# Performance work log

Measured on AMD Instinct MI355X. Metric: run time of the kernel, lower is better.

The kernel has to match this reference:

```python
import jax, jax.numpy as jnp
import numpy as np

NUM_HEADS = 12
HIDDEN = 768
HEAD = HIDDEN // NUM_HEADS
B, N = 16, 512


def setup_inputs() -> dict:
    key = jax.random.key(0)
    ks = jax.random.split(key, 9)
    s = 0.02
    return {
        "x": jax.random.normal(ks[0], (B, N, HIDDEN), jnp.float32),
        "spatial_encoding": jax.random.normal(ks[1], (B, N, N), jnp.float32),
        "edge_encoding": jax.random.normal(ks[2], (B, N, N), jnp.float32),
        "Wq": jax.random.normal(ks[3], (HIDDEN, HIDDEN), jnp.float32) * s,
        "Wk": jax.random.normal(ks[4], (HIDDEN, HIDDEN), jnp.float32) * s,
        "Wv": jax.random.normal(ks[5], (HIDDEN, HIDDEN), jnp.float32) * s,
        "bv": jax.random.normal(ks[6], (HIDDEN,), jnp.float32) * s,
        "Wo": jax.random.normal(ks[7], (HIDDEN, HIDDEN), jnp.float32) * s,
        "bo": jax.random.normal(ks[8], (HIDDEN,), jnp.float32) * s,
    }


def reference(x, spatial_encoding, edge_encoding, Wq, Wk, Wv, bv, Wo, bo):
    b, n, h = x.shape
    scale = jnp.asarray(HIDDEN, x.dtype) ** -0.5  # note: hidden_dim, not head_size
    # projections (torch Linear: x @ W.T + b), split heads -> (b, n, nh, hd)
    q = (x @ Wq.T).reshape(b, n, NUM_HEADS, HEAD)
    k = (x @ Wk.T).reshape(b, n, NUM_HEADS, HEAD)
    v = (x @ Wv.T + bv).reshape(b, n, NUM_HEADS, HEAD)
    bias = (spatial_encoding + edge_encoding)[:, None]  # (b, 1, n, n)
    scores = jnp.einsum("bqhd,bkhd->bhqk", q, k) * scale + bias  # (b, nh, n, n)
    # rows that are entirely zero get masked to -inf, then nan_to_num after softmax
    row_nonzero = jnp.any(scores != 0, axis=-1, keepdims=True)
    scores = jnp.where(row_nonzero, scores, -jnp.inf)
    p = jax.nn.softmax(scores, axis=-1)
    p = jnp.nan_to_num(p)
    out = jnp.einsum("bhqk,bkhd->bqhd", p, v).reshape(b, n, h)
    # dropout is identity in eval mode
    return out @ Wo.T + bo
```

## Files before the change

kernel.cpp:

```cpp
#include <hip/hip_runtime.h>

typedef unsigned short u16;
typedef short bf16x8 __attribute__((ext_vector_type(8)));
typedef short bf16x4 __attribute__((ext_vector_type(4)));
typedef float f32x4 __attribute__((ext_vector_type(4)));
typedef unsigned u32x4 __attribute__((ext_vector_type(4)));
typedef unsigned short u16x4 __attribute__((ext_vector_type(4)));

#define HID 768
#define NH  12
#define HD  64
#define BB  16
#define SEQ 512
#define TOK (BB*SEQ)

static __device__ __forceinline__ u16 f2bf(float f){
  union { float f; unsigned u; } x; x.f = f;
  unsigned r = x.u + 0x7fffu + ((x.u >> 16) & 1u);
  return (u16)(r >> 16);
}
static __device__ __forceinline__ float bf2f(u16 h){
  return __builtin_bit_cast(float, ((unsigned)h) << 16);
}

static __device__ __forceinline__ void gl_lds16(const void* g, void* l){
  __builtin_amdgcn_global_load_lds(
      (const __attribute__((address_space(1))) unsigned int*)g,
      (__attribute__((address_space(3))) unsigned int*)l, 16, 0, 0);
}

__global__ __launch_bounds__(256, 4) void k_convert(
    const float* __restrict__ x,  const float* __restrict__ sp,
    const float* __restrict__ ed, const float* __restrict__ wq,
    const float* __restrict__ wk, const float* __restrict__ wv,
    const float* __restrict__ wo,
    u16* __restrict__ xbf, u16* __restrict__ wqkv, u16* __restrict__ wob,
    u16* __restrict__ bsumb)
{
  const int NQX = TOK*HID/4;
  const int NQW = 3*HID*HID/4;
  const int NQO = HID*HID/4;
  int idx = blockIdx.x*256 + threadIdx.x;
  if (idx < NQX){
    int e = idx*4;
    float4 v = *(const float4*)(x+e);
    ushort4 o; o.x=f2bf(v.x); o.y=f2bf(v.y); o.z=f2bf(v.z); o.w=f2bf(v.w);
    *(ushort4*)(xbf+e) = o;
  } else if (idx < NQX+NQW){
    int e = (idx-NQX)*4;
    int row = e/HID, col = e%HID;
    const float* w = (row<768) ? (wq+row*HID)
                   : (row<1536 ? wk+(row-768)*HID : wv+(row-1536)*HID);
    float4 v = *(const float4*)(w+col);
    ushort4 o; o.x=f2bf(v.x); o.y=f2bf(v.y); o.z=f2bf(v.z); o.w=f2bf(v.w);
    *(ushort4*)(wqkv+e) = o;
  } else if (idx < NQX+NQW+NQO){
    int e = (idx-NQX-NQW)*4;
    float4 v = *(const float4*)(wo+e);
    ushort4 o; o.x=f2bf(v.x); o.y=f2bf(v.y); o.z=f2bf(v.z); o.w=f2bf(v.w);
    *(ushort4*)(wob+e) = o;
  } else {
    int e = (idx-NQX-NQW-NQO)*4;
    float4 a = *(const float4*)(sp+e);
    float4 b = *(const float4*)(ed+e);
    ushort4 o; o.x=f2bf(a.x+b.x); o.y=f2bf(a.y+b.y);
               o.z=f2bf(a.z+b.z); o.w=f2bf(a.w+b.w);
    *(ushort4*)(bsumb+e) = o;
  }
}

template<int MODE>
__global__ __launch_bounds__(256, 2) void k_gemm(
    const u16* __restrict__ A, const u16* __restrict__ Bt,
    const float* __restrict__ bias,
    u16* __restrict__ o16a, u16* __restrict__ o16b,
    float* __restrict__ outf)
{
  __shared__ u16 As[2][128*32];
  __shared__ u16 Bs[2][128*32];
  const int tid = threadIdx.x;
  const int wid = tid >> 6, lane = tid & 63;
  const int g = lane >> 4, c = lane & 15;
  const int wr = wid >> 1, wc = wid & 1;
  const long mbase = (long)blockIdx.y * 128;
  const int  nbase = blockIdx.x * 128;

  f32x4 acc[4][4];
  #pragma unroll
  for (int i=0;i<4;i++)
    #pragma unroll
    for (int j=0;j<4;j++){ f32x4 z = {0.f,0.f,0.f,0.f}; acc[i][j] = z; }

  const char* Abase = (const char*)A  + mbase * HID * 2;
  const char* Bbase = (const char*)Bt + (long)nbase * HID * 2;

  const int L0 = wid*1024 + lane*16;
  const int ar0 = L0 >> 6, ai0 = L0 & 63;
  const int L1 = L0 + 4096;
  const int ar1 = L1 >> 6, ai1 = L1 & 63;

  #define STAGE(buf, kk) do { \
    gl_lds16(Abase + (long)ar0*1536 + (kk)*2 + ai0, (char*)As[buf] + wid*1024); \
    gl_lds16(Abase + (long)ar1*1536 + (kk)*2 + ai1, (char*)As[buf] + 4096 + wid*1024); \
    gl_lds16(Bbase + (long)ar0*1536 + (kk)*2 + ai0, (char*)Bs[buf] + wid*1024); \
    gl_lds16(Bbase + (long)ar1*1536 + (kk)*2 + ai1, (char*)Bs[buf] + 4096 + wid*1024); \
  } while(0)

  STAGE(0, 0);
  __syncthreads();

  #pragma unroll 2
  for (int t = 0; t < 24; t++){
    if (t < 23) STAGE((t+1)&1, (t+1)*32);
    const char* Ab = (const char*)As[t&1];
    const char* Bb = (const char*)Bs[t&1];
    bf16x8 af[4], bfr[4];
    #pragma unroll
    for (int mt=0; mt<4; mt++){
      int row = wr*64 + mt*16 + c;
      af[mt] = *(const bf16x8*)(Ab + row*64 + g*16);
    }
    #pragma unroll
    for (int nt=0; nt<4; nt++){
      int row = wc*64 + nt*16 + c;
      bfr[nt] = *(const bf16x8*)(Bb + row*64 + g*16);
    }
    #pragma unroll
    for (int mt=0; mt<4; mt++)
      #pragma unroll
      for (int nt=0; nt<4; nt++)
        acc[mt][nt] = __builtin_amdgcn_mfma_f32_16x16x32_bf16(
            af[mt], bfr[nt], acc[mt][nt], 0,0,0);
    __syncthreads();
  }
  #undef STAGE

  if constexpr (MODE == 1){
    #pragma unroll
    for (int nt=0; nt<4; nt++){
      int colg = nbase + wc*64 + nt*16 + c;
      float bb = bias[colg];
      #pragma unroll
      for (int mt=0; mt<4; mt++)
        #pragma unroll
        for (int r=0;r<4;r++){
          long rowg = mbase + wr*64 + mt*16 + g*4 + r;
          outf[rowg*HID + colg] = acc[mt][nt][r] + bb;
        }
    }
  } else if constexpr (MODE == 0){
    int region = blockIdx.x / 6;
    #pragma unroll
    for (int nt=0; nt<4; nt++){
      int colg = nbase + wc*64 + nt*16 + c;
      int o = colg - region*768;
      int h = o >> 6, dd = o & 63;
      #pragma unroll
      for (int mt=0; mt<4; mt++)
        #pragma unroll
        for (int r=0;r<4;r++){
          long rowg = mbase + wr*64 + mt*16 + g*4 + r;
          int b = (int)(rowg >> 9), n = (int)(rowg & 511);
          long hb = (long)(b*NH + h);
          u16 val = f2bf(acc[mt][nt][r]);
          if (region==0) o16a[(hb*SEQ + n)*HD + dd] = val;
          else           o16b[(hb*SEQ + n)*HD + dd] = val;
        }
    }
  } else {
    #pragma unroll
    for (int mt=0; mt<4; mt++){
      int rowg0 = (int)mbase + wr*64 + mt*16 + g*4;
      float4 bb = *(const float4*)(bias + rowg0);
      #pragma unroll
      for (int r=0;r<4;r++){
        int rowg = rowg0 + r;
        int h = rowg >> 6, dd = rowg & 63;
        float bv_ = r==0?bb.x : r==1?bb.y : r==2?bb.z : bb.w;
        #pragma unroll
        for (int nt=0; nt<4; nt++){
          int colg = nbase + wc*64 + nt*16 + c;
          int b = colg >> 9, n = colg & 511;
          o16a[((long)(b*NH + h)*HD + dd)*SEQ + n] = f2bf(acc[mt][nt][r] + bv_);
        }
      }
    }
  }
}

__global__ __launch_bounds__(256, 4) void k_attn(
    const u16* __restrict__ Qh, const u16* __restrict__ Kh,
    const u16* __restrict__ VTh, const u16* __restrict__ bsumb,
    u16* __restrict__ attn)
{
  __shared__ u16 Ks[2][64*64];
  __shared__ u16 Vs[2][64*64];

  const int tid = threadIdx.x;
  const int wid = tid>>6, lane = tid&63, g = lane>>4, c = lane&15;
  const int L = (blockIdx.x & 7)*192 + (blockIdx.x >> 3);
  const int qt = L & 7, h = (L>>3) % 12, b = L/96;
  const u16*  Qp = Qh + (long)(b*NH+h)*SEQ*HD;
  const char* Kp = (const char*)(Kh  + (long)(b*NH+h)*SEQ*HD);
  const char* Vp = (const char*)(VTh + (long)(b*NH+h)*HD*SEQ);
  const int qbase = qt*64 + wid*16;

  bf16x8 qf0 = *(const bf16x8*)(Qp + (qbase + c)*HD +  0 + g*8);
  bf16x8 qf1 = *(const bf16x8*)(Qp + (qbase + c)*HD + 32 + g*8);

  const float scale = 0.036084391824351615f;
  const u16* bp = bsumb + (long)b*SEQ*SEQ + (long)(qbase + c)*SEQ + g*4;

  const int s0 = tid*16;
  const int r0 = s0>>7, i0 = (s0&127) ^ ((r0&7)<<4);
  const int s1 = s0 + 4096;
  const int r1 = s1>>7, i1 = (s1&127) ^ ((r1&7)<<4);

  #define STAGE(buf, ch) do { \
    gl_lds16(Kp + (long)((ch)*64 + r0)*128 + i0, (char*)Ks[buf] + wid*1024); \
    gl_lds16(Kp + (long)((ch)*64 + r1)*128 + i1, (char*)Ks[buf] + wid*1024 + 4096); \
    gl_lds16(Vp + (long)r0*1024 + (ch)*128 + i0, (char*)Vs[buf] + wid*1024); \
    gl_lds16(Vp + (long)r1*1024 + (ch)*128 + i1, (char*)Vs[buf] + wid*1024 + 4096); \
  } while(0)

  f32x4 o[4];
  #pragma unroll
  for (int dt=0;dt<4;dt++){ f32x4 z = {0.f,0.f,0.f,0.f}; o[dt]=z; }
  float l = 0.f;

  STAGE(0, 0);
  __syncthreads();

  #pragma unroll
  for (int ch=0; ch<8; ch++){
    if (ch < 7) STAGE((ch+1)&1, ch+1);
    const char* Kb = (const char*)Ks[ch&1];
    const char* Vb = (const char*)Vs[ch&1];
    const u16* bpc = bp + ch*64;
    u16x4 rb0 = *(const u16x4*)(bpc);
    u16x4 rb1 = *(const u16x4*)(bpc + 16);
    u16x4 rb2 = *(const u16x4*)(bpc + 32);
    u16x4 rb3 = *(const u16x4*)(bpc + 48);
    #pragma unroll
    for (int s=0; s<2; s++){
      const u16x4 rA = s ? rb2 : rb0;
      const u16x4 rB = s ? rb3 : rb1;
      const int rAi = s*32 + c, rBi = s*32 + 16 + c;
      const int mA = (rAi&7)<<4, mB = (rBi&7)<<4;
      bf16x8 ka0 = *(const bf16x8*)(Kb + rAi*128 + ((   g*16) ^ mA));
      bf16x8 ka1 = *(const bf16x8*)(Kb + rAi*128 + ((64+g*16) ^ mA));
      bf16x8 kb0 = *(const bf16x8*)(Kb + rBi*128 + ((   g*16) ^ mB));
      bf16x8 kb1 = *(const bf16x8*)(Kb + rBi*128 + ((64+g*16) ^ mB));
      f32x4 sA = {0.f,0.f,0.f,0.f}, sB = {0.f,0.f,0.f,0.f};
      sA = __builtin_amdgcn_mfma_f32_16x16x32_bf16(ka0, qf0, sA, 0,0,0);
      sA = __builtin_amdgcn_mfma_f32_16x16x32_bf16(ka1, qf1, sA, 0,0,0);
      sB = __builtin_amdgcn_mfma_f32_16x16x32_bf16(kb0, qf0, sB, 0,0,0);
      sB = __builtin_amdgcn_mfma_f32_16x16x32_bf16(kb1, qf1, sB, 0,0,0);
      float pA0 = __expf(fmaf(sA[0], scale, bf2f(rA[0])));
      float pA1 = __expf(fmaf(sA[1], scale, bf2f(rA[1])));
      float pA2 = __expf(fmaf(sA[2], scale, bf2f(rA[2])));
      float pA3 = __expf(fmaf(sA[3], scale, bf2f(rA[3])));
      float pB0 = __expf(fmaf(sB[0], scale, bf2f(rB[0])));
      float pB1 = __expf(fmaf(sB[1], scale, bf2f(rB[1])));
      float pB2 = __expf(fmaf(sB[2], scale, bf2f(rB[2])));
      float pB3 = __expf(fmaf(sB[3], scale, bf2f(rB[3])));
      l += ((pA0 + pA1) + (pA2 + pA3)) + ((pB0 + pB1) + (pB2 + pB3));
      u32x4 paw = { (unsigned)f2bf(pA0) | ((unsigned)f2bf(pA1) << 16),
                    (unsigned)f2bf(pA2) | ((unsigned)f2bf(pA3) << 16),
                    (unsigned)f2bf(pB0) | ((unsigned)f2bf(pB1) << 16),
                    (unsigned)f2bf(pB2) | ((unsigned)f2bf(pB3) << 16) };
      bf16x8 pav = __builtin_bit_cast(bf16x8, paw);
      #pragma unroll
      for (int dt=0; dt<4; dt++){
        const int vr = dt*16 + c, mV = (vr&7)<<4;
        bf16x4 v0 = *(const bf16x4*)(Vb + vr*128 + ((s*64    + g*8) ^ mV));
        bf16x4 v1 = *(const bf16x4*)(Vb + vr*128 + ((s*64+32 + g*8) ^ mV));
        bf16x8 vbv = __builtin_shufflevector(v0, v1, 0,1,2,3,4,5,6,7);
        o[dt] = __builtin_amdgcn_mfma_f32_16x16x32_bf16(pav, vbv, o[dt], 0,0,0);
      }
    }
    __syncthreads();
  }
  #undef STAGE

  l += __shfl_xor(l, 16, 64);
  l += __shfl_xor(l, 32, 64);
  float linv = 1.f / l;

  #pragma unroll
  for (int r=0;r<4;r++){
    float li = __shfl(linv, g*4 + r, 64);
    int q = qbase + g*4 + r;
    #pragma unroll
    for (int dt=0; dt<4; dt++)
      attn[(long)(b*SEQ + q)*HID + h*64 + dt*16 + c] = f2bf(o[dt][r] * li);
  }
}

extern "C" void kernel_launch(void* const* d_in, const int* in_sizes, int n_in,
                              void* d_out, int out_size, void* d_ws, size_t ws_size,
                              hipStream_t stream)
{
  const float* x  = (const float*)d_in[0];
  const float* sp = (const float*)d_in[1];
  const float* ed = (const float*)d_in[2];
  const float* Wq = (const float*)d_in[3];
  const float* Wk = (const float*)d_in[4];
  const float* Wv = (const float*)d_in[5];
  const float* bv = (const float*)d_in[6];
  const float* Wo = (const float*)d_in[7];
  const float* bo = (const float*)d_in[8];
  float* out = (float*)d_out;

  u16* w = (u16*)d_ws;
  u16* xbf  = w;
  u16* wqkv = xbf  + TOK*HID;
  u16* wob  = wqkv + 3*HID*HID;
  u16* qh   = wob  + HID*HID;
  u16* kh   = qh   + TOK*HID;
  u16* vth  = kh   + TOK*HID;
  u16* attn = vth  + TOK*HID;
  u16* bsumb = attn + TOK*HID;

  k_convert<<<12544, 256, 0, stream>>>(x, sp, ed, Wq, Wk, Wv, Wo,
                                       xbf, wqkv, wob, bsumb);
  dim3 gQK(12, 64);
  k_gemm<0><<<gQK, 256, 0, stream>>>(xbf, wqkv, nullptr, qh, kh, nullptr);
  dim3 gVT(64, 6);
  k_gemm<2><<<gVT, 256, 0, stream>>>(wqkv + 2*HID*HID, xbf, bv, vth, nullptr, nullptr);
  k_attn<<<1536, 256, 0, stream>>>(qh, kh, vth, bsumb, attn);
  dim3 gO(6, 64);
  k_gemm<1><<<gO, 256, 0, stream>>>(attn, wob, bo, nullptr, nullptr, out);
}
```

Baseline: 146.7 us.

## Process two query tiles per attention block to reuse K/V LDS tiles

Each attention block now handles 128 query rows instead of 64, with each wave computing two 16-row query groups that share the same K and V fragments loaded from LDS. This halves the number of blocks and halves the global K/V staging traffic per query, and it amortizes the LDS reads across twice the MFMA work. In exchange it raises register pressure, so launch bounds drop to 3 blocks per CU, and with 768 blocks there is less parallelism to hide latency.

New measurement: 155.3 us. 1.06x slower.

```diff
diff --git a/kernel.cpp b/kernel.cpp
--- a/kernel.cpp
+++ b/kernel.cpp
@@ -188,7 +188,7 @@
   }
 }
 
-__global__ __launch_bounds__(256, 4) void k_attn(
+__global__ __launch_bounds__(256, 3) void k_attn(
     const u16* __restrict__ Qh, const u16* __restrict__ Kh,
     const u16* __restrict__ VTh, const u16* __restrict__ bsumb,
     u16* __restrict__ attn)
@@ -198,18 +198,22 @@
 
   const int tid = threadIdx.x;
   const int wid = tid>>6, lane = tid&63, g = lane>>4, c = lane&15;
-  const int L = (blockIdx.x & 7)*192 + (blockIdx.x >> 3);
-  const int qt = L & 7, h = (L>>3) % 12, b = L/96;
+  const int L = (blockIdx.x & 7)*96 + (blockIdx.x >> 3);
+  const int qt2 = L & 3, h = (L>>2) % 12, b = L/48;
   const u16*  Qp = Qh + (long)(b*NH+h)*SEQ*HD;
   const char* Kp = (const char*)(Kh  + (long)(b*NH+h)*SEQ*HD);
   const char* Vp = (const char*)(VTh + (long)(b*NH+h)*HD*SEQ);
-  const int qbase = qt*64 + wid*16;
-
-  bf16x8 qf0 = *(const bf16x8*)(Qp + (qbase + c)*HD +  0 + g*8);
-  bf16x8 qf1 = *(const bf16x8*)(Qp + (qbase + c)*HD + 32 + g*8);
+  const int qb0 = qt2*128 + wid*16;
+  const int qb1 = qb0 + 64;
+
+  bf16x8 qA0 = *(const bf16x8*)(Qp + (qb0 + c)*HD +  0 + g*8);
+  bf16x8 qA1 = *(const bf16x8*)(Qp + (qb0 + c)*HD + 32 + g*8);
+  bf16x8 qB0 = *(const bf16x8*)(Qp + (qb1 + c)*HD +  0 + g*8);
+  bf16x8 qB1 = *(const bf16x8*)(Qp + (qb1 + c)*HD + 32 + g*8);
 
   const float scale = 0.036084391824351615f;
-  const u16* bp = bsumb + (long)b*SEQ*SEQ + (long)(qbase + c)*SEQ + g*4;
+  const u16* bp0 = bsumb + (long)b*SEQ*SEQ + (long)(qb0 + c)*SEQ + g*4;
+  const u16* bp1 = bp0 + 64*SEQ;
 
   const int s0 = tid*16;
   const int r0 = s0>>7, i0 = (s0&127) ^ ((r0&7)<<4);
@@ -223,10 +227,10 @@
     gl_lds16(Vp + (long)r1*1024 + (ch)*128 + i1, (char*)Vs[buf] + wid*1024 + 4096); \
   } while(0)
 
-  f32x4 o[4];
+  f32x4 o0[4], o1[4];
   #pragma unroll
-  for (int dt=0;dt<4;dt++){ f32x4 z = {0.f,0.f,0.f,0.f}; o[dt]=z; }
-  float l = 0.f;
+  for (int dt=0;dt<4;dt++){ f32x4 z = {0.f,0.f,0.f,0.f}; o0[dt]=z; o1[dt]=z; }
+  float l0 = 0.f, l1 = 0.f;
 
   STAGE(0, 0);
   __syncthreads();
@@ -236,64 +240,92 @@
     if (ch < 7) STAGE((ch+1)&1, ch+1);
     const char* Kb = (const char*)Ks[ch&1];
     const char* Vb = (const char*)Vs[ch&1];
-    const u16* bpc = bp + ch*64;
-    u16x4 rb0 = *(const u16x4*)(bpc);
-    u16x4 rb1 = *(const u16x4*)(bpc + 16);
-    u16x4 rb2 = *(const u16x4*)(bpc + 32);
-    u16x4 rb3 = *(const u16x4*)(bpc + 48);
+    const u16* bpc0 = bp0 + ch*64;
+    const u16* bpc1 = bp1 + ch*64;
+    u16x4 ra0 = *(const u16x4*)(bpc0);      u16x4 ra1 = *(const u16x4*)(bpc0+16);
+    u16x4 ra2 = *(const u16x4*)(bpc0+32);   u16x4 ra3 = *(const u16x4*)(bpc0+48);
+    u16x4 rc0 = *(const u16x4*)(bpc1);      u16x4 rc1 = *(const u16x4*)(bpc1+16);
+    u16x4 rc2 = *(const u16x4*)(bpc1+32);   u16x4 rc3 = *(const u16x4*)(bpc1+48);
     #pragma unroll
     for (int s=0; s<2; s++){
-      const u16x4 rA = s ? rb2 : rb0;
-      const u16x4 rB = s ? rb3 : rb1;
+      const u16x4 bA0 = s ? ra2 : ra0;
+      const u16x4 bB0 = s ? ra3 : ra1;
+      const u16x4 bA1 = s ? rc2 : rc0;
+      const u16x4 bB1 = s ? rc3 : rc1;
       const int rAi = s*32 + c, rBi = s*32 + 16 + c;
       const int mA = (rAi&7)<<4, mB = (rBi&7)<<4;
       bf16x8 ka0 = *(const bf16x8*)(Kb + rAi*128 + ((   g*16) ^ mA));
       bf16x8 ka1 = *(const bf16x8*)(Kb + rAi*128 + ((64+g*16) ^ mA));
       bf16x8 kb0 = *(const bf16x8*)(Kb + rBi*128 + ((   g*16) ^ mB));
       bf16x8 kb1 = *(const bf16x8*)(Kb + rBi*128 + ((64+g*16) ^ mB));
-      f32x4 sA = {0.f,0.f,0.f,0.f}, sB = {0.f,0.f,0.f,0.f};
-      sA = __builtin_amdgcn_mfma_f32_16x16x32_bf16(ka0, qf0, sA, 0,0,0);
-      sA = __builtin_amdgcn_mfma_f32_16x16x32_bf16(ka1, qf1, sA, 0,0,0);
-      sB = __builtin_amdgcn_mfma_f32_16x16x32_bf16(kb0, qf0, sB, 0,0,0);
-      sB = __builtin_amdgcn_mfma_f32_16x16x32_bf16(kb1, qf1, sB, 0,0,0);
-      float pA0 = __expf(fmaf(sA[0], scale, bf2f(rA[0])));
-      float pA1 = __expf(fmaf(sA[1], scale, bf2f(rA[1])));
-      float pA2 = __expf(fmaf(sA[2], scale, bf2f(rA[2])));
-      float pA3 = __expf(fmaf(sA[3], scale, bf2f(rA[3])));
-      float pB0 = __expf(fmaf(sB[0], scale, bf2f(rB[0])));
-      float pB1 = __expf(fmaf(sB[1], scale, bf2f(rB[1])));
-      float pB2 = __expf(fmaf(sB[2], scale, bf2f(rB[2])));
-      float pB3 = __expf(fmaf(sB[3], scale, bf2f(rB[3])));
-      l += ((pA0 + pA1) + (pA2 + pA3)) + ((pB0 + pB1) + (pB2 + pB3));
-      u32x4 paw = { (unsigned)f2bf(pA0) | ((unsigned)f2bf(pA1) << 16),
+      f32x4 sA0={0.f,0.f,0.f,0.f}, sB0={0.f,0.f,0.f,0.f};
+      f32x4 sA1={0.f,0.f,0.f,0.f}, sB1={0.f,0.f,0.f,0.f};
+      sA0 = __builtin_amdgcn_mfma_f32_16x16x32_bf16(ka0, qA0, sA0, 0,0,0);
+      sA0 = __builtin_amdgcn_mfma_f32_16x16x32_bf16(ka1, qA1, sA0, 0,0,0);
+      sB0 = __builtin_amdgcn_mfma_f32_16x16x32_bf16(kb0, qA0, sB0, 0,0,0);
+      sB0 = __builtin_amdgcn_mfma_f32_16x16x32_bf16(kb1, qA1, sB0, 0,0,0);
+      sA1 = __builtin_amdgcn_mfma_f32_16x16x32_bf16(ka0, qB0, sA1, 0,0,0);
+      sA1 = __builtin_amdgcn_mfma_f32_16x16x32_bf16(ka1, qB1, sA1, 0,0,0);
+      sB1 = __builtin_amdgcn_mfma_f32_16x16x32_bf16(kb0, qB0, sB1, 0,0,0);
+      sB1 = __builtin_amdgcn_mfma_f32_16x16x32_bf16(kb1, qB1, sB1, 0,0,0);
+      float pA0 = __expf(fmaf(sA0[0], scale, bf2f(bA0[0])));
+      float pA1 = __expf(fmaf(sA0[1], scale, bf2f(bA0[1])));
+      float pA2 = __expf(fmaf(sA0[2], scale, bf2f(bA0[2])));
+      float pA3 = __expf(fmaf(sA0[3], scale, bf2f(bA0[3])));
+      float pB0 = __expf(fmaf(sB0[0], scale, bf2f(bB0[0])));
+      float pB1 = __expf(fmaf(sB0[1], scale, bf2f(bB0[1])));
+      float pB2 = __expf(fmaf(sB0[2], scale, bf2f(bB0[2])));
+      float pB3 = __expf(fmaf(sB0[3], scale, bf2f(bB0[3])));
+      l0 += ((pA0 + pA1) + (pA2 + pA3)) + ((pB0 + pB1) + (pB2 + pB3));
+      u32x4 pw0 = { (unsigned)f2bf(pA0) | ((unsigned)f2bf(pA1) << 16),
                     (unsigned)f2bf(pA2) | ((unsigned)f2bf(pA3) << 16),
                     (unsigned)f2bf(pB0) | ((unsigned)f2bf(pB1) << 16),
                     (unsigned)f2bf(pB2) | ((unsigned)f2bf(pB3) << 16) };
-      bf16x8 pav = __builtin_bit_cast(bf16x8, paw);
+      bf16x8 pav0 = __builtin_bit_cast(bf16x8, pw0);
+      float qA0f = __expf(fmaf(sA1[0], scale, bf2f(bA1[0])));
+      float qA1f = __expf(fmaf(sA1[1], scale, bf2f(bA1[1])));
+      float qA2f = __expf(fmaf(sA1[2], scale, bf2f(bA1[2])));
+      float qA3f = __expf(fmaf(sA1[3], scale, bf2f(bA1[3])));
+      float qB0f = __expf(fmaf(sB1[0], scale, bf2f(bB1[0])));
+      float qB1f = __expf(fmaf(sB1[1], scale, bf2f(bB1[1])));
+      float qB2f = __expf(fmaf(sB1[2], scale, bf2f(bB1[2])));
+      float qB3f = __expf(fmaf(sB1[3], scale, bf2f(bB1[3])));
+      l1 += ((qA0f + qA1f) + (qA2f + qA3f)) + ((qB0f + qB1f) + (qB2f + qB3f));
+      u32x4 pw1 = { (unsigned)f2bf(qA0f) | ((unsigned)f2bf(qA1f) << 16),
+                    (unsigned)f2bf(qA2f) | ((unsigned)f2bf(qA3f) << 16),
+                    (unsigned)f2bf(qB0f) | ((unsigned)f2bf(qB1f) << 16),
+                    (unsigned)f2bf(qB2f) | ((unsigned)f2bf(qB3f) << 16) };
+      bf16x8 pav1 = __builtin_bit_cast(bf16x8, pw1);
       #pragma unroll
       for (int dt=0; dt<4; dt++){
         const int vr = dt*16 + c, mV = (vr&7)<<4;
         bf16x4 v0 = *(const bf16x4*)(Vb + vr*128 + ((s*64    + g*8) ^ mV));
         bf16x4 v1 = *(const bf16x4*)(Vb + vr*128 + ((s*64+32 + g*8) ^ mV));
         bf16x8 vbv = __builtin_shufflevector(v0, v1, 0,1,2,3,4,5,6,7);
-        o[dt] = __builtin_amdgcn_mfma_f32_16x16x32_bf16(pav, vbv, o[dt], 0,0,0);
+        o0[dt] = __builtin_amdgcn_mfma_f32_16x16x32_bf16(pav0, vbv, o0[dt], 0,0,0);
+        o1[dt] = __builtin_amdgcn_mfma_f32_16x16x32_bf16(pav1, vbv, o1[dt], 0,0,0);
       }
     }
     __syncthreads();
   }
   #undef STAGE
 
-  l += __shfl_xor(l, 16, 64);
-  l += __shfl_xor(l, 32, 64);
-  float linv = 1.f / l;
+  l0 += __shfl_xor(l0, 16, 64);
+  l0 += __shfl_xor(l0, 32, 64);
+  l1 += __shfl_xor(l1, 16, 64);
+  l1 += __shfl_xor(l1, 32, 64);
+  float li0 = 1.f / l0, li1 = 1.f / l1;
 
   #pragma unroll
   for (int r=0;r<4;r++){
-    float li = __shfl(linv, g*4 + r, 64);
-    int q = qbase + g*4 + r;
-    #pragma unroll
-    for (int dt=0; dt<4; dt++)
-      attn[(long)(b*SEQ + q)*HID + h*64 + dt*16 + c] = f2bf(o[dt][r] * li);
+    float u0 = __shfl(li0, g*4 + r, 64);
+    float u1 = __shfl(li1, g*4 + r, 64);
+    int q0 = qb0 + g*4 + r, q1 = qb1 + g*4 + r;
+    #pragma unroll
+    for (int dt=0; dt<4; dt++){
+      attn[(long)(b*SEQ + q0)*HID + h*64 + dt*16 + c] = f2bf(o0[dt][r] * u0);
+      attn[(long)(b*SEQ + q1)*HID + h*64 + dt*16 + c] = f2bf(o1[dt][r] * u1);
+    }
   }
 }
 
@@ -328,7 +360,7 @@
   k_gemm<0><<<gQK, 256, 0, stream>>>(xbf, wqkv, nullptr, qh, kh, nullptr);
   dim3 gVT(64, 6);
   k_gemm<2><<<gVT, 256, 0, stream>>>(wqkv + 2*HID*HID, xbf, bv, vth, nullptr, nullptr);
-  k_attn<<<1536, 256, 0, stream>>>(qh, kh, vth, bsumb, attn);
+  k_attn<<<768, 256, 0, stream>>>(qh, kh, vth, bsumb, attn);
   dim3 gO(6, 64);
   k_gemm<1><<<gO, 256, 0, stream>>>(attn, wob, bo, nullptr, nullptr, out);
 }
```

## Triple-buffer K/V/bias tiles in LDS with async loads and fine-grained waits

Applied to the files above, without the earlier changes.

The attention kernel now moves from double to triple buffering of K and V tiles. It also stages the bias tile through LDS with async global-to-LDS copies instead of per-lane direct global loads. Full __syncthreads is replaced by explicit vmcnt waits plus s_barrier, and MFMA sections get raised wave priority through s_setprio. The aim is to hide global memory latency two chunks ahead and overlap waves better, at the cost of more LDS use per block. The launch-bounds occupancy hint drops from 4 to 2.

Result: faster. 125.9 us (-14.2%).

```diff
diff --git a/kernel.cpp b/kernel.cpp
--- a/kernel.cpp
+++ b/kernel.cpp
@@ -188,13 +188,14 @@
   }
 }
 
-__global__ __launch_bounds__(256, 4) void k_attn(
+__global__ __launch_bounds__(256, 2) void k_attn(
     const u16* __restrict__ Qh, const u16* __restrict__ Kh,
     const u16* __restrict__ VTh, const u16* __restrict__ bsumb,
     u16* __restrict__ attn)
 {
-  __shared__ u16 Ks[2][64*64];
-  __shared__ u16 Vs[2][64*64];
+  __shared__ u16 Ks[3][4096];
+  __shared__ u16 Vs[3][4096];
+  __shared__ u16 Bs[3][4096];
 
   const int tid = threadIdx.x;
   const int wid = tid>>6, lane = tid&63, g = lane>>4, c = lane&15;
@@ -203,13 +204,13 @@
   const u16*  Qp = Qh + (long)(b*NH+h)*SEQ*HD;
   const char* Kp = (const char*)(Kh  + (long)(b*NH+h)*SEQ*HD);
   const char* Vp = (const char*)(VTh + (long)(b*NH+h)*HD*SEQ);
+  const char* Bp = (const char*)(bsumb + (long)b*SEQ*SEQ + (long)(qt*64)*SEQ);
   const int qbase = qt*64 + wid*16;
 
   bf16x8 qf0 = *(const bf16x8*)(Qp + (qbase + c)*HD +  0 + g*8);
   bf16x8 qf1 = *(const bf16x8*)(Qp + (qbase + c)*HD + 32 + g*8);
 
   const float scale = 0.036084391824351615f;
-  const u16* bp = bsumb + (long)b*SEQ*SEQ + (long)(qbase + c)*SEQ + g*4;
 
   const int s0 = tid*16;
   const int r0 = s0>>7, i0 = (s0&127) ^ ((r0&7)<<4);
@@ -221,7 +222,11 @@
     gl_lds16(Kp + (long)((ch)*64 + r1)*128 + i1, (char*)Ks[buf] + wid*1024 + 4096); \
     gl_lds16(Vp + (long)r0*1024 + (ch)*128 + i0, (char*)Vs[buf] + wid*1024); \
     gl_lds16(Vp + (long)r1*1024 + (ch)*128 + i1, (char*)Vs[buf] + wid*1024 + 4096); \
+    gl_lds16(Bp + (long)r0*1024 + (ch)*128 + i0, (char*)Bs[buf] + wid*1024); \
+    gl_lds16(Bp + (long)r1*1024 + (ch)*128 + i1, (char*)Bs[buf] + wid*1024 + 4096); \
   } while(0)
+
+  #define VMW(n) asm volatile("s_waitcnt vmcnt(" #n ")" ::: "memory")
 
   f32x4 o[4];
   #pragma unroll
@@ -229,18 +234,21 @@
   float l = 0.f;
 
   STAGE(0, 0);
-  __syncthreads();
+  STAGE(1, 1);
+  VMW(6);
+  __builtin_amdgcn_s_barrier();
 
   #pragma unroll
   for (int ch=0; ch<8; ch++){
-    if (ch < 7) STAGE((ch+1)&1, ch+1);
-    const char* Kb = (const char*)Ks[ch&1];
-    const char* Vb = (const char*)Vs[ch&1];
-    const u16* bpc = bp + ch*64;
-    u16x4 rb0 = *(const u16x4*)(bpc);
-    u16x4 rb1 = *(const u16x4*)(bpc + 16);
-    u16x4 rb2 = *(const u16x4*)(bpc + 32);
-    u16x4 rb3 = *(const u16x4*)(bpc + 48);
+    if (ch < 6) STAGE((ch+2)%3, ch+2);
+    const char* Kb = (const char*)Ks[ch%3];
+    const char* Vb = (const char*)Vs[ch%3];
+    const char* Bb = (const char*)Bs[ch%3];
+    const int brow = wid*16 + c, mBs = (c&7)<<4;
+    u16x4 rb0 = *(const u16x4*)(Bb + brow*128 + (( 0 + g*8) ^ mBs));
+    u16x4 rb1 = *(const u16x4*)(Bb + brow*128 + ((32 + g*8) ^ mBs));
+    u16x4 rb2 = *(const u16x4*)(Bb + brow*128 + ((64 + g*8) ^ mBs));
+    u16x4 rb3 = *(const u16x4*)(Bb + brow*128 + ((96 + g*8) ^ mBs));
     #pragma unroll
     for (int s=0; s<2; s++){
       const u16x4 rA = s ? rb2 : rb0;
@@ -252,10 +260,12 @@
       bf16x8 kb0 = *(const bf16x8*)(Kb + rBi*128 + ((   g*16) ^ mB));
       bf16x8 kb1 = *(const bf16x8*)(Kb + rBi*128 + ((64+g*16) ^ mB));
       f32x4 sA = {0.f,0.f,0.f,0.f}, sB = {0.f,0.f,0.f,0.f};
+      __builtin_amdgcn_s_setprio(1);
       sA = __builtin_amdgcn_mfma_f32_16x16x32_bf16(ka0, qf0, sA, 0,0,0);
       sA = __builtin_amdgcn_mfma_f32_16x16x32_bf16(ka1, qf1, sA, 0,0,0);
       sB = __builtin_amdgcn_mfma_f32_16x16x32_bf16(kb0, qf0, sB, 0,0,0);
       sB = __builtin_amdgcn_mfma_f32_16x16x32_bf16(kb1, qf1, sB, 0,0,0);
+      __builtin_amdgcn_s_setprio(0);
       float pA0 = __expf(fmaf(sA[0], scale, bf2f(rA[0])));
       float pA1 = __expf(fmaf(sA[1], scale, bf2f(rA[1])));
       float pA2 = __expf(fmaf(sA[2], scale, bf2f(rA[2])));
@@ -270,6 +280,7 @@
                     (unsigned)f2bf(pB0) | ((unsigned)f2bf(pB1) << 16),
                     (unsigned)f2bf(pB2) | ((unsigned)f2bf(pB3) << 16) };
       bf16x8 pav = __builtin_bit_cast(bf16x8, paw);
+      __builtin_amdgcn_s_setprio(1);
       #pragma unroll
       for (int dt=0; dt<4; dt++){
         const int vr = dt*16 + c, mV = (vr&7)<<4;
@@ -278,10 +289,14 @@
         bf16x8 vbv = __builtin_shufflevector(v0, v1, 0,1,2,3,4,5,6,7);
         o[dt] = __builtin_amdgcn_mfma_f32_16x16x32_bf16(pav, vbv, o[dt], 0,0,0);
       }
-    }
-    __syncthreads();
+      __builtin_amdgcn_s_setprio(0);
+    }
+    if (ch < 6)      VMW(6);
+    else if (ch == 6) VMW(0);
+    if (ch < 7) __builtin_amdgcn_s_barrier();
   }
   #undef STAGE
+  #undef VMW
 
   l += __shfl_xor(l, 16, 64);
   l += __shfl_xor(l, 32, 64);
```
